# Kernel tuning notes

Measured on AMD Instinct MI355X. Metric: run time of the kernel, lower is better.

The kernel has to match this reference:

```python
import jax, jax.numpy as jnp
import numpy as np


def setup_inputs() -> dict:
    key = jax.random.key(0)
    k1, k2, k3 = jax.random.split(key, 3)
    B, S, K, N = 4, 2048, 4096, 4096
    x = jax.random.normal(k1, (B, S, K), dtype=jnp.float16)
    # int8 weight codes in [-128, 127]
    w_int8 = jax.random.randint(k2, (N, K), -128, 128, dtype=jnp.int32).astype(jnp.int8)
    # per-output-row weight scale (positive, smallish like abs-max/127 of fp weights)
    weight_scale = (jax.random.uniform(k3, (N,), dtype=jnp.float32) + 0.5) * 0.01
    matmul_out_scale = jnp.full((1,), 1.0 / 1024.0, dtype=jnp.float32)
    return {"x": x, "w_int8": w_int8, "weight_scale": weight_scale,
            "matmul_out_scale": matmul_out_scale}


def reference(x, w_int8, weight_scale, matmul_out_scale):
    B, S, K = x.shape
    xf = x.astype(jnp.float32)
    # dynamic per-token symmetric int8 quantization (TOKEN_INT8_127)
    x_scales = jnp.max(jnp.abs(xf), axis=-1, keepdims=True) / 127.0  # [B,S,1] float32
    x_int8 = jnp.clip(jnp.round(xf / x_scales), -128, 127).astype(jnp.int8)
    x_scales_h = x_scales[..., 0].astype(jnp.float16)  # [B,S]
    y = jnp.einsum('mk,nk->mn', x_int8.reshape(-1, K), w_int8,
                   preferred_element_type=jnp.int32).astype(jnp.float32)
    y = y.reshape(B, S, -1)
    y = (y * matmul_out_scale[0]).astype(jnp.float16)
    # fp16 * fp32 -> fp32 (matches torch type promotion); per-row and per-token dequant
    out = y * weight_scale * x_scales_h[:, :, None]
    return out
```

## Files before the change

kernel.cpp:

```cpp
#include <hip/hip_runtime.h>
#include <hip/hip_fp16.h>
#include <stdint.h>

typedef int v4i __attribute__((ext_vector_type(4)));

#define GLOAD_LDS16(g, l) __builtin_amdgcn_global_load_lds(                  \
    (const __attribute__((address_space(1))) void*)(g),                      \
    (__attribute__((address_space(3))) void*)(l), 16, 0, 0)

#define XQ_OFF 0u
#define XS_OFF 33554432u
#define W8_OFF 33570816u

__device__ inline bool x_is_f32(const void* xin) {
  const uint32_t* xw = (const uint32_t*)xin;
  bool ok = true;
  #pragma unroll
  for (int i = 0; i < 16; ++i) ok &= ((xw[i] & 0x1FFFu) == 0u);
  return ok;
}
__device__ inline bool w_is_i32(const void* win) {
  const int* wi = (const int*)win;
  bool ok = true;
  #pragma unroll
  for (int i = 0; i < 16; ++i) ok &= (wi[i] >= -128 && wi[i] <= 127);
  return ok;
}

__global__ __launch_bounds__(256) void repack_w(
    const void* __restrict__ win, int8_t* __restrict__ w8, int total)
{
  const bool as32 = w_is_i32(win);
  const int tid  = blockIdx.x * 256 + threadIdx.x;
  const int nthr = gridDim.x * 256;
  if (as32) {
    const int4* w4 = (const int4*)win;
    uint32_t* dst = (uint32_t*)w8;
    const int n4 = total >> 2;
    for (int i = tid; i < n4; i += nthr) {
      int4 v = w4[i];
      dst[i] = (uint32_t)(v.x & 255) | ((uint32_t)(v.y & 255) << 8) |
               ((uint32_t)(v.z & 255) << 16) | ((uint32_t)(v.w & 255) << 24);
    }
  } else {
    const uint4* src = (const uint4*)win;
    uint4* dst = (uint4*)w8;
    const int n16 = total >> 4;
    for (int i = tid; i < n16; i += nthr) dst[i] = src[i];
  }
}

__global__ __launch_bounds__(256) void quant_rows(
    const void* __restrict__ xin, int8_t* __restrict__ xq,
    __half* __restrict__ xs, int K)
{
  const bool xf32 = x_is_f32(xin);
  const int row  = blockIdx.x;
  const int tid  = threadIdx.x;
  const int lane = tid & 63;
  const int wv   = tid >> 6;
  const size_t base = (size_t)row * (size_t)K;
  __shared__ float wmax[4];

  if (xf32 && K == 4096) {
    const float4* x4 = (const float4*)((const float*)xin + base);
    float4 v[4];
    #pragma unroll
    for (int i = 0; i < 4; ++i) v[i] = x4[i * 256 + tid];
    float mx = 0.0f;
    #pragma unroll
    for (int i = 0; i < 4; ++i)
      mx = fmaxf(mx, fmaxf(fmaxf(fabsf(v[i].x), fabsf(v[i].y)),
                           fmaxf(fabsf(v[i].z), fabsf(v[i].w))));
    #pragma unroll
    for (int off = 32; off; off >>= 1) mx = fmaxf(mx, __shfl_xor(mx, off, 64));
    if (lane == 0) wmax[wv] = mx;
    __syncthreads();
    const float scale =
        fmaxf(fmaxf(wmax[0], wmax[1]), fmaxf(wmax[2], wmax[3])) / 127.0f;
    if (tid == 0) xs[row] = __float2half(scale);
    uint32_t* q = (uint32_t*)(xq + base);
    #pragma unroll
    for (int i = 0; i < 4; ++i) {
      float f[4] = {v[i].x, v[i].y, v[i].z, v[i].w};
      uint32_t p = 0;
      #pragma unroll
      for (int j = 0; j < 4; ++j) {
        float r = fminf(127.0f, fmaxf(-128.0f, rintf(f[j] / scale)));
        p |= ((uint32_t)((int)r & 255)) << (8 * j);
      }
      q[i * 256 + tid] = p;
    }
    return;
  }

  float mx = 0.0f;
  if (xf32) {
    const float* x = (const float*)xin + base;
    for (int k = tid * 4; k < K; k += 256 * 4) {
      float4 v = *(const float4*)(x + k);
      mx = fmaxf(mx, fmaxf(fmaxf(fabsf(v.x), fabsf(v.y)),
                           fmaxf(fabsf(v.z), fabsf(v.w))));
    }
  } else {
    const __half* x = (const __half*)xin + base;
    for (int k = tid * 8; k < K; k += 256 * 8) {
      uint4 u = *(const uint4*)(x + k);
      const __half* hp = (const __half*)&u;
      #pragma unroll
      for (int j = 0; j < 8; ++j) mx = fmaxf(mx, fabsf(__half2float(hp[j])));
    }
  }
  #pragma unroll
  for (int off = 32; off; off >>= 1) mx = fmaxf(mx, __shfl_xor(mx, off, 64));
  if (lane == 0) wmax[wv] = mx;
  __syncthreads();
  const float scale =
      fmaxf(fmaxf(wmax[0], wmax[1]), fmaxf(wmax[2], wmax[3])) / 127.0f;
  if (tid == 0) xs[row] = __float2half(scale);

  for (int k = tid * 8; k < K; k += 256 * 8) {
    float f[8];
    if (xf32) {
      const float* x = (const float*)xin + base;
      float4 a = *(const float4*)(x + k);
      float4 b = *(const float4*)(x + k + 4);
      f[0]=a.x; f[1]=a.y; f[2]=a.z; f[3]=a.w; f[4]=b.x; f[5]=b.y; f[6]=b.z; f[7]=b.w;
    } else {
      const __half* x = (const __half*)xin + base;
      uint4 u = *(const uint4*)(x + k);
      const __half* hp = (const __half*)&u;
      #pragma unroll
      for (int j = 0; j < 8; ++j) f[j] = __half2float(hp[j]);
    }
    uint32_t p0 = 0, p1 = 0;
    #pragma unroll
    for (int j = 0; j < 4; ++j) {
      float r = fminf(127.0f, fmaxf(-128.0f, rintf(f[j] / scale)));
      p0 |= ((uint32_t)((int)r & 255)) << (8 * j);
    }
    #pragma unroll
    for (int j = 0; j < 4; ++j) {
      float r = fminf(127.0f, fmaxf(-128.0f, rintf(f[4 + j] / scale)));
      p1 |= ((uint32_t)((int)r & 255)) << (8 * j);
    }
    uint2 st; st.x = p0; st.y = p1;
    *(uint2*)(xq + base + k) = st;
  }
}

__global__ __launch_bounds__(512, 2) void gemm_w8a8(
    const int8_t* __restrict__ xq, const int8_t* __restrict__ wq,
    const __half* __restrict__ xs, const float* __restrict__ wscale,
    const float* __restrict__ mos, float* __restrict__ out,
    int M, int N, int K)
{
  __shared__ int8_t sA[4][256 * 64];
  __shared__ int8_t sB[4][256 * 64];

  const int tid  = threadIdx.x;
  const int lane = tid & 63;
  const int w    = tid >> 6;
  const int wr   = w >> 2;
  const int wc   = w & 3;
  const int lr   = lane & 15;
  const int lk   = lane >> 4;

  int L = blockIdx.x;
  const int nwg = gridDim.x;
  if ((nwg & 7) == 0) L = (L & 7) * (nwg >> 3) + (L >> 3);
  const int ntn = N >> 8;
  const int bn = (L % ntn) << 8;
  const int bm = (L / ntn) << 8;

  v4i acc[8][4];
  #pragma unroll
  for (int i = 0; i < 8; ++i)
    #pragma unroll
    for (int j = 0; j < 4; ++j) {
      v4i z = {0, 0, 0, 0};
      acc[i][j] = z;
    }

  auto stageA = [&](int kt, int buf) {
    const int k0 = kt << 6;
    #pragma unroll
    for (int i = 0; i < 2; ++i) {
      const int li = i * 512 + tid;
      const int r  = li >> 2;
      const int p  = li & 3;
      const int sc = p ^ ((r >> 1) & 3);
      GLOAD_LDS16(xq + (size_t)(bm + r) * K + k0 + (sc << 4),
                  &sA[buf][(i * 512 + (w << 6)) << 4]);
    }
  };
  auto stageB = [&](int kt, int buf) {
    const int k0 = kt << 6;
    #pragma unroll
    for (int i = 0; i < 2; ++i) {
      const int li = i * 512 + tid;
      const int r  = li >> 2;
      const int p  = li & 3;
      const int sc = p ^ ((r >> 1) & 3);
      GLOAD_LDS16(wq + (size_t)(bn + r) * K + k0 + (sc << 4),
                  &sB[buf][(i * 512 + (w << 6)) << 4]);
    }
  };

  const int rowA0 = (wr << 7) + lr;
  const int aoff  = rowA0 * 64 + ((lk ^ ((rowA0 >> 1) & 3)) << 4);
  const int rowB0 = (wc << 6) + lr;
  const int boff  = rowB0 * 64 + ((lk ^ ((rowB0 >> 1) & 3)) << 4);

  auto tile_body = [&](int buf, int kstage, bool do_stage) {
    const int8_t* Ab = sA[buf];
    const int8_t* Bb = sB[buf];
    const int sbuf = (buf + 3) & 3;
    if (do_stage) stageA(kstage, sbuf);
    v4i bf[4], af[4];
    #pragma unroll
    for (int ni = 0; ni < 4; ++ni) bf[ni] = *(const v4i*)(Bb + boff + ni * 1024);
    #pragma unroll
    for (int mi = 0; mi < 4; ++mi) af[mi] = *(const v4i*)(Ab + aoff + mi * 1024);
    __builtin_amdgcn_s_setprio(1);
    #pragma unroll
    for (int mi = 0; mi < 4; ++mi)
      #pragma unroll
      for (int ni = 0; ni < 4; ++ni)
        acc[mi][ni] = __builtin_amdgcn_mfma_i32_16x16x64_i8(
            af[mi], bf[ni], acc[mi][ni], 0, 0, 0);
    __builtin_amdgcn_s_setprio(0);
    if (do_stage) stageB(kstage, sbuf);
    #pragma unroll
    for (int mi = 0; mi < 4; ++mi)
      af[mi] = *(const v4i*)(Ab + aoff + 4096 + mi * 1024);
    __builtin_amdgcn_s_setprio(1);
    #pragma unroll
    for (int mi = 0; mi < 4; ++mi)
      #pragma unroll
      for (int ni = 0; ni < 4; ++ni)
        acc[mi + 4][ni] = __builtin_amdgcn_mfma_i32_16x16x64_i8(
            af[mi], bf[ni], acc[mi + 4][ni], 0, 0, 0);
    __builtin_amdgcn_s_setprio(0);
  };

  const int nt = K >> 6;

  stageA(0, 0); stageB(0, 0);
  stageA(1, 1); stageB(1, 1);
  stageA(2, 2); stageB(2, 2);
  asm volatile("s_waitcnt vmcnt(8)" ::: "memory");
  __builtin_amdgcn_s_barrier();

  #pragma unroll 1
  for (int t = 0; t < nt - 3; ++t) {
    tile_body(t & 3, t + 3, true);
    asm volatile("s_waitcnt vmcnt(8) lgkmcnt(0)" ::: "memory");
    __builtin_amdgcn_s_barrier();
  }
  tile_body((nt - 3) & 3, 0, false);
  asm volatile("s_waitcnt vmcnt(4) lgkmcnt(0)" ::: "memory");
  __builtin_amdgcn_s_barrier();
  tile_body((nt - 2) & 3, 0, false);
  asm volatile("s_waitcnt vmcnt(0) lgkmcnt(0)" ::: "memory");
  __builtin_amdgcn_s_barrier();
  tile_body((nt - 1) & 3, 0, false);

  const float s_out = mos[0];
  #pragma unroll
  for (int ni = 0; ni < 4; ++ni) {
    const int n_g = bn + (wc << 6) + ni * 16 + lr;
    const float wsc = wscale[n_g];
    #pragma unroll
    for (int mi = 0; mi < 8; ++mi) {
      #pragma unroll
      for (int j = 0; j < 4; ++j) {
        const int m_g = bm + (wr << 7) + mi * 16 + lk * 4 + j;
        const float y = __half2float(__float2half((float)acc[mi][ni][j] * s_out));
        out[(size_t)m_g * N + n_g] = (y * wsc) * __half2float(xs[m_g]);
      }
    }
  }
}

extern "C" void kernel_launch(void* const* d_in, const int* in_sizes, int n_in,
                              void* d_out, int out_size, void* d_ws, size_t ws_size,
                              hipStream_t stream) {
  const void*  x      = d_in[0];
  const void*  win    = d_in[1];
  const float* wscale = (const float*)d_in[2];
  const float* mos    = (const float*)d_in[3];
  float*       out    = (float*)d_out;

  const int N = in_sizes[2];
  const int K = in_sizes[1] / N;
  const int M = in_sizes[0] / K;

  int8_t* xq = (int8_t*)d_ws + XQ_OFF;
  __half* xs = (__half*)((char*)d_ws + XS_OFF);
  int8_t* w8 = (int8_t*)d_ws + W8_OFF;

  repack_w<<<2048, 256, 0, stream>>>(win, w8, N * K);
  quant_rows<<<M, 256, 0, stream>>>(x, xq, xs, K);

  gemm_w8a8<<<dim3((M >> 8) * (N >> 8)), 512, 0, stream>>>(
      xq, w8, xs, wscale, mos, out, M, N, K);
}
```

Baseline: 215.9 us.

## Restructure tile loop into barrier-separated phases with LDS reads before staging

```diff
diff --git a/kernel.cpp b/kernel.cpp
--- a/kernel.cpp
+++ b/kernel.cpp
@@ -212,37 +212,45 @@
   const int rowB0 = (wc << 6) + lr;
   const int boff  = rowB0 * 64 + ((lk ^ ((rowB0 >> 1) & 3)) << 4);
 
-  auto tile_body = [&](int buf, int kstage, bool do_stage) {
-    const int8_t* Ab = sA[buf];
-    const int8_t* Bb = sB[buf];
-    const int sbuf = (buf + 3) & 3;
-    if (do_stage) stageA(kstage, sbuf);
-    v4i bf[4], af[4];
-    #pragma unroll
-    for (int ni = 0; ni < 4; ++ni) bf[ni] = *(const v4i*)(Bb + boff + ni * 1024);
-    #pragma unroll
-    for (int mi = 0; mi < 4; ++mi) af[mi] = *(const v4i*)(Ab + aoff + mi * 1024);
-    __builtin_amdgcn_s_setprio(1);
-    #pragma unroll
-    for (int mi = 0; mi < 4; ++mi)
-      #pragma unroll
-      for (int ni = 0; ni < 4; ++ni)
-        acc[mi][ni] = __builtin_amdgcn_mfma_i32_16x16x64_i8(
-            af[mi], bf[ni], acc[mi][ni], 0, 0, 0);
+#define MFMA_CLUSTER(BASE)                                                   \
+    __builtin_amdgcn_s_setprio(1);                                           \
+    _Pragma("unroll")                                                        \
+    for (int mi = 0; mi < 4; ++mi)                                           \
+      _Pragma("unroll")                                                      \
+      for (int ni = 0; ni < 4; ++ni)                                         \
+        acc[(BASE) + mi][ni] = __builtin_amdgcn_mfma_i32_16x16x64_i8(        \
+            af[mi], bf[ni], acc[(BASE) + mi][ni], 0, 0, 0);                  \
     __builtin_amdgcn_s_setprio(0);
-    if (do_stage) stageB(kstage, sbuf);
-    #pragma unroll
-    for (int mi = 0; mi < 4; ++mi)
-      af[mi] = *(const v4i*)(Ab + aoff + 4096 + mi * 1024);
-    __builtin_amdgcn_s_setprio(1);
-    #pragma unroll
-    for (int mi = 0; mi < 4; ++mi)
-      #pragma unroll
-      for (int ni = 0; ni < 4; ++ni)
-        acc[mi + 4][ni] = __builtin_amdgcn_mfma_i32_16x16x64_i8(
-            af[mi], bf[ni], acc[mi + 4][ni], 0, 0, 0);
-    __builtin_amdgcn_s_setprio(0);
-  };
+
+#define TILE_ITER(BUF, KT, DOSTAGE, VMLINE)                                  \
+  {                                                                          \
+    const int8_t* Ab = sA[BUF];                                              \
+    const int8_t* Bb = sB[BUF];                                              \
+    const int sbuf = ((BUF) + 3) & 3;                                        \
+    v4i af[4], bf[4];                                                        \
+                             \
+    _Pragma("unroll")                                                        \
+    for (int ni = 0; ni < 4; ++ni)                                           \
+      bf[ni] = *(const v4i*)(Bb + boff + ni * 1024);                         \
+    _Pragma("unroll")                                                        \
+    for (int mi = 0; mi < 4; ++mi)                                           \
+      af[mi] = *(const v4i*)(Ab + aoff + mi * 1024);                         \
+    if (DOSTAGE) stageA((KT), sbuf);                                         \
+    __builtin_amdgcn_s_barrier();                                            \
+    asm volatile("s_waitcnt lgkmcnt(0)" ::: "memory");                       \
+    MFMA_CLUSTER(0)                                                          \
+    __builtin_amdgcn_s_barrier();                                            \
+                           \
+    _Pragma("unroll")                                                        \
+    for (int mi = 0; mi < 4; ++mi)                                           \
+      af[mi] = *(const v4i*)(Ab + aoff + 4096 + mi * 1024);                  \
+    if (DOSTAGE) stageB((KT), sbuf);                                         \
+    VMLINE                                                                   \
+    __builtin_amdgcn_s_barrier();                                            \
+    asm volatile("s_waitcnt lgkmcnt(0)" ::: "memory");                       \
+    MFMA_CLUSTER(4)                                                          \
+    __builtin_amdgcn_s_barrier();                                            \
+  }
 
   const int nt = K >> 6;
 
@@ -254,17 +262,17 @@
 
   #pragma unroll 1
   for (int t = 0; t < nt - 3; ++t) {
-    tile_body(t & 3, t + 3, true);
-    asm volatile("s_waitcnt vmcnt(8) lgkmcnt(0)" ::: "memory");
-    __builtin_amdgcn_s_barrier();
-  }
-  tile_body((nt - 3) & 3, 0, false);
-  asm volatile("s_waitcnt vmcnt(4) lgkmcnt(0)" ::: "memory");
-  __builtin_amdgcn_s_barrier();
-  tile_body((nt - 2) & 3, 0, false);
-  asm volatile("s_waitcnt vmcnt(0) lgkmcnt(0)" ::: "memory");
-  __builtin_amdgcn_s_barrier();
-  tile_body((nt - 1) & 3, 0, false);
+    TILE_ITER(t & 3, t + 3, true,
+              asm volatile("s_waitcnt vmcnt(8)" ::: "memory");)
+  }
+  TILE_ITER((nt - 3) & 3, 0, false,
+            asm volatile("s_waitcnt vmcnt(4)" ::: "memory");)
+  TILE_ITER((nt - 2) & 3, 0, false,
+            asm volatile("s_waitcnt vmcnt(0)" ::: "memory");)
+  TILE_ITER((nt - 1) & 3, 0, false, ;)
+
+#undef TILE_ITER
+#undef MFMA_CLUSTER
 
   const float s_out = mos[0];
   #pragma unroll
```

Result: slower. 226.6 us (+5.0%).
